# Kernel tuning notes

Measured on AMD Instinct MI355X. Metric: run time of the kernel, lower is better.

Reference implementation:

```python
import jax, jax.numpy as jnp
import numpy as np

G = 4      # deformable groups
K = 9      # 3x3 kernel points
EPS = 1e-5


def _bilinear_gather(value, loc_y, loc_x):
    # value: (N,H,W,G,Cg); loc_*: (N,H,W,G,K) float pixel coords, zero padding outside.
    N, H, W, g, Cg = value.shape
    y0f = jnp.floor(loc_y); x0f = jnp.floor(loc_x)
    wy = loc_y - y0f; wx = loc_x - x0f
    y0 = y0f.astype(jnp.int32); x0 = x0f.astype(jnp.int32)
    n_idx = jnp.arange(N).reshape(N, 1, 1, 1, 1)
    g_idx = jnp.arange(g).reshape(1, 1, 1, g, 1)

    def corner(yi, xi, w):
        valid = (yi >= 0) & (yi < H) & (xi >= 0) & (xi < W)
        yc = jnp.clip(yi, 0, H - 1); xc = jnp.clip(xi, 0, W - 1)
        v = value[n_idx, yc, xc, g_idx]  # (N,H,W,G,K,Cg) irregular gather
        return v * (w * valid)[..., None]

    return (corner(y0, x0, (1 - wy) * (1 - wx))
            + corner(y0, x0 + 1, (1 - wy) * wx)
            + corner(y0 + 1, x0, wy * (1 - wx))
            + corner(y0 + 1, x0 + 1, wy * wx))


def _dcnv4(t, H, W, Wv, bv, Wom, bom, Wo):
    # DCNv4 on (N,L,C): value proj -> learned-offset bilinear sampling with
    # UNNORMALIZED dynamic weights (no softmax, DCNv4) -> output proj (no bias).
    N, L, C = t.shape
    Cg = C // G
    value = (t @ Wv + bv).reshape(N, H, W, G, Cg)
    om = (t @ Wom + bom).reshape(N, H, W, G, 3 * K)
    offset = om[..., :2 * K].reshape(N, H, W, G, K, 2)  # (dx, dy) per point
    mask = om[..., 2 * K:]                               # (N,H,W,G,K)
    ky, kx = jnp.meshgrid(jnp.arange(-1, 2), jnp.arange(-1, 2), indexing='ij')
    ky = ky.reshape(-1).astype(t.dtype); kx = kx.reshape(-1).astype(t.dtype)
    ys = jnp.arange(H, dtype=t.dtype).reshape(1, H, 1, 1, 1)
    xs = jnp.arange(W, dtype=t.dtype).reshape(1, 1, W, 1, 1)
    loc_y = ys + ky + offset[..., 1]  # (N,H,W,G,K)
    loc_x = xs + kx + offset[..., 0]
    sampled = _bilinear_gather(value, loc_y, loc_x)  # (N,H,W,G,K,Cg)
    out = (sampled * mask[..., None]).sum(axis=4)    # (N,H,W,G,Cg)
    return out.reshape(N, L, C) @ Wo


def _bn(x, gamma, beta):
    # training-mode BatchNorm2d: per-channel batch stats over (N,H,W)
    mean = x.mean(axis=(0, 2, 3), keepdims=True)
    var = ((x - mean) ** 2).mean(axis=(0, 2, 3), keepdims=True)
    return (x - mean) * jax.lax.rsqrt(var + EPS) * gamma.reshape(1, -1, 1, 1) \
        + beta.reshape(1, -1, 1, 1)


def setup_inputs() -> dict:
    key = jax.random.key(0)
    ks = jax.random.split(key, 6)
    N, C, H, W = 4, 128, 64, 64
    s = 1.0 / np.sqrt(C)
    x = jax.random.normal(ks[0], (N, C, H, W), jnp.float32)
    Wv = jax.random.normal(ks[1], (C, C), jnp.float32) * s      # value_proj
    bv = jnp.zeros((C,), jnp.float32)
    Wom = jax.random.normal(ks[2], (C, G * 3 * K), jnp.float32) * 0.01  # offset+mask head
    bom = jnp.zeros((G * 3 * K,), jnp.float32)
    Wo = jax.random.normal(ks[3], (C, C), jnp.float32) * s      # output_proj (bias=False)
    gamma = jnp.ones((C,), jnp.float32)
    beta = jnp.zeros((C,), jnp.float32)
    Wc = jax.random.normal(ks[4], (C, C), jnp.float32) * s      # 1x1 conv (out=in=C)
    return {"x": x, "Wv": Wv, "bv": bv, "Wom": Wom, "bom": bom,
            "Wo": Wo, "gamma": gamma, "beta": beta, "Wc": Wc}


def reference(x, Wv, bv, Wom, bom, Wo, gamma, beta, Wc):
    N, C, H, W = x.shape
    shortcut = x
    t = x.transpose(0, 2, 3, 1).reshape(N, H * W, C)
    t = _dcnv4(t, H, W, Wv, bv, Wom, bom, Wo)
    y = t.reshape(N, H, W, C).transpose(0, 3, 1, 2)
    y = jax.nn.relu(_bn(y, gamma, beta))
    t = y.transpose(0, 2, 3, 1).reshape(N, H * W, C)
    t = _dcnv4(t, H, W, Wv, bv, Wom, bom, Wo)  # same DCNv4 weights reused
    y = t.reshape(N, H, W, C).transpose(0, 3, 1, 2)
    y = _bn(y, gamma, beta)                    # same BN params reused, no relu here
    y = y + shortcut                           # in_channels == out_channels
    return jnp.einsum('nchw,oc->nohw', y, Wc)  # final 1x1 conv
```

## Files before the change

kernel.cpp:

```cpp
#include <hip/hip_runtime.h>
#include <math.h>

#define CC   128
#define NL   16384
#define OMP  112
#define HH   64
#define WW   64

typedef __attribute__((ext_vector_type(8))) short short8;
typedef __attribute__((ext_vector_type(4))) float f32x4;

__device__ __forceinline__ unsigned short f2bf(float f) {
    union { float f; unsigned u; } v; v.f = f;
    unsigned r = v.u + 0x7fff + ((v.u >> 16) & 1);
    return (unsigned short)(r >> 16);
}
__device__ __forceinline__ float bf2f(unsigned short u) {
    union { unsigned u; float f; } v; v.u = ((unsigned)u) << 16;
    return v.f;
}

__global__ __launch_bounds__(256) void prep_kernel(
    const float* __restrict__ Wv, const float* __restrict__ Wom,
    const float* __restrict__ Wo, const float* __restrict__ Wc,
    unsigned short* __restrict__ Wcomb, unsigned short* __restrict__ WoT,
    unsigned short* __restrict__ Wcb, float* __restrict__ stats)
{
    int tid = threadIdx.x;
    int b   = blockIdx.x;
    if (b < 16) stats[b * 256 + tid] = 0.0f;
    int i = b * 256 + tid;
    if (i < 32768) {
        int r = i >> 7, k = i & 127;
        unsigned short v;
        if (r < 128)      v = f2bf(Wv[k * CC + r]);
        else if (r < 240) { int nn = r - 128; v = (nn < 108) ? f2bf(Wom[k * 108 + nn]) : (unsigned short)0; }
        else              v = 0;
        Wcomb[i] = v;
    } else if (i < 49152) {
        int j = i - 32768; int nn = j >> 7, k = j & 127;
        WoT[j] = f2bf(Wo[k * CC + nn]);
    } else {
        int j = i - 49152;
        Wcb[j] = f2bf(Wc[j]);
    }
}

template<int IN_MODE>
__global__ __launch_bounds__(256) void gemm_vom_kernel(
    const float* __restrict__ Ain, const unsigned short* __restrict__ Wcomb,
    const float* __restrict__ bv, const float* __restrict__ bom,
    const float* __restrict__ stats, const float* __restrict__ gamma,
    const float* __restrict__ beta,
    unsigned short* __restrict__ val, float* __restrict__ omb)
{
    __shared__ unsigned short As[16 * 136];
    __shared__ float bnsc[128], bnsh[128];

    int tid = threadIdx.x;
    int block_m = blockIdx.x * 16;

    if (IN_MODE == 1) {
        if (tid < 128) {
            float s = 0.0f, sq = 0.0f;
#pragma unroll
            for (int g = 0; g < 8; g++) {
                s  += stats[g * 256 + tid];
                sq += stats[g * 256 + 128 + tid];
            }
            const float inv = 1.0f / 16384.0f;
            float mean = s * inv;
            float var  = sq * inv - mean * mean;
            float sc   = rsqrtf(var + 1e-5f) * gamma[tid];
            bnsc[tid] = sc;
            bnsh[tid] = beta[tid] - mean * sc;
        }
        __syncthreads();
    }

    if (IN_MODE == 0) {
        int n   = block_m >> 12;
        int hw0 = block_m & 4095;
#pragma unroll
        for (int i = 0; i < 2; i++) {
            int id = tid + i * 256;
            int c  = id >> 2, j4 = id & 3;
            float4 v = *(const float4*)(Ain + (((size_t)(n * CC + c)) << 12) + hw0 + j4 * 4);
            As[(j4 * 4 + 0) * 136 + c] = f2bf(v.x);
            As[(j4 * 4 + 1) * 136 + c] = f2bf(v.y);
            As[(j4 * 4 + 2) * 136 + c] = f2bf(v.z);
            As[(j4 * 4 + 3) * 136 + c] = f2bf(v.w);
        }
    } else {
#pragma unroll
        for (int i = 0; i < 2; i++) {
            int id = tid + i * 256;
            int r  = id >> 5, c = (id & 31) * 4;
            float4 v = *(const float4*)(Ain + (size_t)(block_m + r) * CC + c);
            As[r * 136 + c + 0] = f2bf(fmaxf(v.x * bnsc[c + 0] + bnsh[c + 0], 0.0f));
            As[r * 136 + c + 1] = f2bf(fmaxf(v.y * bnsc[c + 1] + bnsh[c + 1], 0.0f));
            As[r * 136 + c + 2] = f2bf(fmaxf(v.z * bnsc[c + 2] + bnsh[c + 2], 0.0f));
            As[r * 136 + c + 3] = f2bf(fmaxf(v.w * bnsc[c + 3] + bnsh[c + 3], 0.0f));
        }
    }
    __syncthreads();

    int w  = tid >> 6;
    int l  = tid & 63;
    int lr = l & 15, lk = l >> 4;

    f32x4 acc[4];
#pragma unroll
    for (int nt = 0; nt < 4; nt++) acc[nt] = (f32x4){0.f, 0.f, 0.f, 0.f};

#pragma unroll
    for (int kk = 0; kk < 4; kk++) {
        short8 a = *(const short8*)(&As[lr * 136 + kk * 32 + lk * 8]);
#pragma unroll
        for (int nt = 0; nt < 4; nt++) {
            int ntile = w + nt * 4;
            short8 b = *(const short8*)(Wcomb + (size_t)(ntile * 16 + lr) * CC + kk * 32 + lk * 8);
            acc[nt] = __builtin_amdgcn_mfma_f32_16x16x32_bf16(a, b, acc[nt], 0, 0, 0);
        }
    }

    int row0 = block_m + lk * 4;
#pragma unroll
    for (int nt = 0; nt < 4; nt++) {
        int col = (w + nt * 4) * 16 + lr;
        if (col < 128) {
            float bb = bv[col];
#pragma unroll
            for (int r = 0; r < 4; r++)
                val[(size_t)(row0 + r) * CC + col] = f2bf(acc[nt][r] + bb);
        } else if (col < 240) {
            int oc = col - 128;
            float bb = (oc < 108) ? bom[oc] : 0.0f;
#pragma unroll
            for (int r = 0; r < 4; r++)
                omb[(size_t)(row0 + r) * OMP + oc] = acc[nt][r] + bb;
        }
    }
}

__global__ __launch_bounds__(256) void sample_kernel(
    const unsigned short* __restrict__ val, const float* __restrict__ omb,
    unsigned int* __restrict__ sbuf)
{
    int tid    = threadIdx.x;
    int gid    = blockIdx.x * 256 + tid;
    int unit   = gid >> 4;
    int lane16 = gid & 15;
    int nl = unit >> 2;
    int g  = unit & 3;
    int n  = nl >> 12;
    int hw = nl & 4095;
    int h  = hw >> 6;
    int w  = hw & 63;

    const float* omp = omb + (size_t)nl * OMP + g * 27;
    const unsigned short* vb = val + (((size_t)n) << 19) + g * 32 + lane16 * 2;

    float acc0 = 0.0f, acc1 = 0.0f;
#pragma unroll
    for (int k = 0; k < 9; k++) {
        float ox = omp[2 * k];
        float oy = omp[2 * k + 1];
        float mk = omp[18 + k];
        float ly = (float)(h + k / 3 - 1) + oy;
        float lx = (float)(w + k % 3 - 1) + ox;
        float y0f = floorf(ly), x0f = floorf(lx);
        float wy = ly - y0f, wx = lx - x0f;
        int y0 = (int)y0f, x0 = (int)x0f;

        float v0 = 0.0f, v1 = 0.0f;
#pragma unroll
        for (int cy = 0; cy < 2; cy++) {
#pragma unroll
            for (int cx = 0; cx < 2; cx++) {
                int yi = y0 + cy, xi = x0 + cx;
                float wgt = (cy ? wy : 1.0f - wy) * (cx ? wx : 1.0f - wx);
                bool valid = (yi >= 0) && (yi < HH) && (xi >= 0) && (xi < WW);
                wgt = valid ? wgt : 0.0f;
                int yc = min(max(yi, 0), HH - 1);
                int xc = min(max(xi, 0), WW - 1);
                unsigned int pv = *(const unsigned int*)(vb + (size_t)(yc * WW + xc) * CC);
                v0 += bf2f((unsigned short)(pv & 0xffff)) * wgt;
                v1 += bf2f((unsigned short)(pv >> 16)) * wgt;
            }
        }
        acc0 += mk * v0;
        acc1 += mk * v1;
    }
    unsigned int packed = (unsigned int)f2bf(acc0) | ((unsigned int)f2bf(acc1) << 16);
    sbuf[(size_t)nl * 64 + g * 16 + lane16] = packed;
}

__global__ __launch_bounds__(256) void gemm_o_bn_kernel(
    const unsigned short* __restrict__ A, const unsigned short* __restrict__ Bt,
    float* __restrict__ ybuf, float* __restrict__ stats)
{
    __shared__ float lstat[256];
    int tid = threadIdx.x;
    int block_m = blockIdx.x * 16;
    lstat[tid] = 0.0f;
    __syncthreads();

    int w  = tid >> 6;
    int l  = tid & 63;
    int lr = l & 15, lk = l >> 4;

    f32x4 acc[2];
    acc[0] = (f32x4){0.f, 0.f, 0.f, 0.f};
    acc[1] = (f32x4){0.f, 0.f, 0.f, 0.f};

#pragma unroll
    for (int kk = 0; kk < 4; kk++) {
        short8 a = *(const short8*)(A + (size_t)(block_m + lr) * CC + kk * 32 + lk * 8);
#pragma unroll
        for (int nt = 0; nt < 2; nt++) {
            short8 b = *(const short8*)(Bt + (size_t)((w * 2 + nt) * 16 + lr) * CC + kk * 32 + lk * 8);
            acc[nt] = __builtin_amdgcn_mfma_f32_16x16x32_bf16(a, b, acc[nt], 0, 0, 0);
        }
    }

    int row0 = block_m + lk * 4;
#pragma unroll
    for (int nt = 0; nt < 2; nt++) {
        int col = (w * 2 + nt) * 16 + lr;
        float s = 0.0f, sq = 0.0f;
#pragma unroll
        for (int r = 0; r < 4; r++) {
            float v = acc[nt][r];
            ybuf[(size_t)(row0 + r) * CC + col] = v;
            s += v;
            sq += v * v;
        }
        atomicAdd(&lstat[col], s);
        atomicAdd(&lstat[128 + col], sq);
    }
    __syncthreads();
    if (tid < 128) {
        float* sg = stats + (blockIdx.x & 7) * 256;
        atomicAdd(&sg[tid], lstat[tid]);
        atomicAdd(&sg[128 + tid], lstat[128 + tid]);
    }
}

__global__ __launch_bounds__(256) void gemm_final_kernel(
    const float* __restrict__ ybuf, const float* __restrict__ x,
    const unsigned short* __restrict__ Bt, const float* __restrict__ stats,
    const float* __restrict__ gamma, const float* __restrict__ beta,
    float* __restrict__ out)
{
    __shared__ unsigned short As[16 * 136];
    __shared__ float Xs[16 * 132];
    __shared__ float T[128 * 20];
    __shared__ float bnsc[128], bnsh[128];

    int tid = threadIdx.x;
    int block_m = blockIdx.x * 16;
    int n   = block_m >> 12;
    int hw0 = block_m & 4095;

    if (tid < 128) {
        float s = 0.0f, sq = 0.0f;
#pragma unroll
        for (int g = 0; g < 8; g++) {
            s  += stats[g * 256 + tid];
            sq += stats[g * 256 + 128 + tid];
        }
        const float inv = 1.0f / 16384.0f;
        float mean = s * inv;
        float var  = sq * inv - mean * mean;
        float sc   = rsqrtf(var + 1e-5f) * gamma[tid];
        bnsc[tid] = sc;
        bnsh[tid] = beta[tid] - mean * sc;
    }

#pragma unroll
    for (int i = 0; i < 2; i++) {
        int id = tid + i * 256;
        int c  = id >> 2, j4 = id & 3;
        float4 v = *(const float4*)(x + (((size_t)(n * CC + c)) << 12) + hw0 + j4 * 4);
        Xs[(j4 * 4 + 0) * 132 + c] = v.x;
        Xs[(j4 * 4 + 1) * 132 + c] = v.y;
        Xs[(j4 * 4 + 2) * 132 + c] = v.z;
        Xs[(j4 * 4 + 3) * 132 + c] = v.w;
    }
    __syncthreads();

#pragma unroll
    for (int i = 0; i < 2; i++) {
        int id = tid + i * 256;
        int r  = id >> 5, c = (id & 31) * 4;
        float4 v = *(const float4*)(ybuf + (size_t)(block_m + r) * CC + c);
        As[r * 136 + c + 0] = f2bf(v.x * bnsc[c + 0] + bnsh[c + 0] + Xs[r * 132 + c + 0]);
        As[r * 136 + c + 1] = f2bf(v.y * bnsc[c + 1] + bnsh[c + 1] + Xs[r * 132 + c + 1]);
        As[r * 136 + c + 2] = f2bf(v.z * bnsc[c + 2] + bnsh[c + 2] + Xs[r * 132 + c + 2]);
        As[r * 136 + c + 3] = f2bf(v.w * bnsc[c + 3] + bnsh[c + 3] + Xs[r * 132 + c + 3]);
    }
    __syncthreads();

    int w  = tid >> 6;
    int l  = tid & 63;
    int lr = l & 15, lk = l >> 4;

    f32x4 acc[2];
    acc[0] = (f32x4){0.f, 0.f, 0.f, 0.f};
    acc[1] = (f32x4){0.f, 0.f, 0.f, 0.f};

#pragma unroll
    for (int kk = 0; kk < 4; kk++) {
        short8 a = *(const short8*)(&As[lr * 136 + kk * 32 + lk * 8]);
#pragma unroll
        for (int nt = 0; nt < 2; nt++) {
            short8 b = *(const short8*)(Bt + (size_t)((w * 2 + nt) * 16 + lr) * CC + kk * 32 + lk * 8);
            acc[nt] = __builtin_amdgcn_mfma_f32_16x16x32_bf16(a, b, acc[nt], 0, 0, 0);
        }
    }

#pragma unroll
    for (int nt = 0; nt < 2; nt++) {
        int col = (w * 2 + nt) * 16 + lr;
#pragma unroll
        for (int r = 0; r < 4; r++)
            T[col * 20 + lk * 4 + r] = acc[nt][r];
    }
    __syncthreads();
#pragma unroll
    for (int i = 0; i < 2; i++) {
        int id = tid + i * 256;
        int o  = id >> 2, j4 = id & 3;
        float4 v = *(const float4*)(&T[o * 20 + j4 * 4]);
        *(float4*)(out + (((size_t)(n * CC + o)) << 12) + hw0 + j4 * 4) = v;
    }
}

extern "C" void kernel_launch(void* const* d_in, const int* in_sizes, int n_in,
                              void* d_out, int out_size, void* d_ws, size_t ws_size,
                              hipStream_t stream)
{
    const float* x     = (const float*)d_in[0];
    const float* Wv    = (const float*)d_in[1];
    const float* bv    = (const float*)d_in[2];
    const float* Wom   = (const float*)d_in[3];
    const float* bom   = (const float*)d_in[4];
    const float* Wo    = (const float*)d_in[5];
    const float* gamma = (const float*)d_in[6];
    const float* beta  = (const float*)d_in[7];
    const float* Wc    = (const float*)d_in[8];
    float* out = (float*)d_out;

    char* ws = (char*)d_ws;
    unsigned short* val   = (unsigned short*)ws;   ws += (size_t)NL * CC * 2;
    float*          omb   = (float*)ws;            ws += (size_t)NL * OMP * 4;
    unsigned int*   sbuf  = (unsigned int*)ws;     ws += (size_t)NL * CC * 2;
    float*          ybuf  = (float*)ws;            ws += (size_t)NL * CC * 4;
    unsigned short* Wcomb = (unsigned short*)ws;   ws += 256 * 128 * 2;
    unsigned short* WoT   = (unsigned short*)ws;   ws += 128 * 128 * 2;
    unsigned short* Wcb   = (unsigned short*)ws;   ws += 128 * 128 * 2;
    float*          stats = (float*)ws;            ws += 4096 * 4;

    dim3 b256(256);

    prep_kernel<<<256, b256, 0, stream>>>(Wv, Wom, Wo, Wc, Wcomb, WoT, Wcb, stats);

    gemm_vom_kernel<0><<<1024, b256, 0, stream>>>(x, Wcomb, bv, bom,
                                                  nullptr, nullptr, nullptr, val, omb);
    sample_kernel<<<4096, b256, 0, stream>>>(val, omb, sbuf);
    gemm_o_bn_kernel<<<1024, b256, 0, stream>>>((const unsigned short*)sbuf, WoT, ybuf, stats);

    gemm_vom_kernel<1><<<1024, b256, 0, stream>>>(ybuf, Wcomb, bv, bom,
                                                  stats, gamma, beta, val, omb);
    sample_kernel<<<4096, b256, 0, stream>>>(val, omb, sbuf);
    gemm_o_bn_kernel<<<1024, b256, 0, stream>>>((const unsigned short*)sbuf, WoT, ybuf, stats + 2048);

    gemm_final_kernel<<<1024, b256, 0, stream>>>(ybuf, x, Wcb, stats + 2048, gamma, beta, out);
}
```

Before: 167.9 us.

## Fuse sampling with output GEMM, enlarge tiles, stage weights in LDS per block

Removes the separate weight-prep kernel: each block now converts Wv/Wom/Wo/Wc to bf16 into shared memory itself. The bilinear sampling kernel is fused with the output projection GEMM and BN statistics, so the intermediate sampled buffer never goes through global memory. Row tiles grow from 16 to 64, cutting the grid to 256 blocks, and each sampling thread now handles 8 channels with 16-byte loads. This saves launches and global traffic, but each block repeats the weight conversion and uses a lot of LDS, which lowers occupancy and parallelism (256 blocks across many CUs).

```diff
diff --git a/kernel.cpp b/kernel.cpp
--- a/kernel.cpp
+++ b/kernel.cpp
@@ -3,7 +3,6 @@
 
 #define CC   128
 #define NL   16384
-#define OMP  112
 #define HH   64
 #define WW   64
 
@@ -20,53 +19,32 @@
     return v.f;
 }
 
-__global__ __launch_bounds__(256) void prep_kernel(
-    const float* __restrict__ Wv, const float* __restrict__ Wom,
-    const float* __restrict__ Wo, const float* __restrict__ Wc,
-    unsigned short* __restrict__ Wcomb, unsigned short* __restrict__ WoT,
-    unsigned short* __restrict__ Wcb, float* __restrict__ stats)
-{
-    int tid = threadIdx.x;
-    int b   = blockIdx.x;
-    if (b < 16) stats[b * 256 + tid] = 0.0f;
-    int i = b * 256 + tid;
-    if (i < 32768) {
-        int r = i >> 7, k = i & 127;
-        unsigned short v;
-        if (r < 128)      v = f2bf(Wv[k * CC + r]);
-        else if (r < 240) { int nn = r - 128; v = (nn < 108) ? f2bf(Wom[k * 108 + nn]) : (unsigned short)0; }
-        else              v = 0;
-        Wcomb[i] = v;
-    } else if (i < 49152) {
-        int j = i - 32768; int nn = j >> 7, k = j & 127;
-        WoT[j] = f2bf(Wo[k * CC + nn]);
-    } else {
-        int j = i - 49152;
-        Wcb[j] = f2bf(Wc[j]);
-    }
-}
-
 template<int IN_MODE>
 __global__ __launch_bounds__(256) void gemm_vom_kernel(
-    const float* __restrict__ Ain, const unsigned short* __restrict__ Wcomb,
-    const float* __restrict__ bv, const float* __restrict__ bom,
-    const float* __restrict__ stats, const float* __restrict__ gamma,
-    const float* __restrict__ beta,
-    unsigned short* __restrict__ val, float* __restrict__ omb)
+    const float* __restrict__ Ain, const float* __restrict__ Wv,
+    const float* __restrict__ bv, const float* __restrict__ Wom,
+    const float* __restrict__ bom, const float* __restrict__ stats_in,
+    const float* __restrict__ gamma, const float* __restrict__ beta,
+    unsigned short* __restrict__ val, float* __restrict__ omb,
+    float* __restrict__ stats_zero)
 {
-    __shared__ unsigned short As[16 * 136];
+    __shared__ unsigned short As[64 * 136];
+    __shared__ unsigned short Bs[128 * 136];
     __shared__ float bnsc[128], bnsh[128];
 
-    int tid = threadIdx.x;
-    int block_m = blockIdx.x * 16;
-
-    if (IN_MODE == 1) {
+    const int tid = threadIdx.x;
+    const int bid = blockIdx.x;
+    const int block_m = bid * 64;
+
+    if (IN_MODE == 0) {
+        if (bid < 16) stats_zero[bid * 256 + tid] = 0.0f;
+    } else {
         if (tid < 128) {
-            float s = 0.0f, sq = 0.0f;
+            float s = 0.f, sq = 0.f;
 #pragma unroll
             for (int g = 0; g < 8; g++) {
-                s  += stats[g * 256 + tid];
-                sq += stats[g * 256 + 128 + tid];
+                s  += stats_in[g * 256 + tid];
+                sq += stats_in[g * 256 + 128 + tid];
             }
             const float inv = 1.0f / 16384.0f;
             float mean = s * inv;
@@ -79,13 +57,13 @@
     }
 
     if (IN_MODE == 0) {
-        int n   = block_m >> 12;
-        int hw0 = block_m & 4095;
-#pragma unroll
-        for (int i = 0; i < 2; i++) {
+        int n_img = block_m >> 12;
+        int hw0   = block_m & 4095;
+#pragma unroll
+        for (int i = 0; i < 8; i++) {
             int id = tid + i * 256;
-            int c  = id >> 2, j4 = id & 3;
-            float4 v = *(const float4*)(Ain + (((size_t)(n * CC + c)) << 12) + hw0 + j4 * 4);
+            int c = id >> 4, j4 = id & 15;
+            float4 v = *(const float4*)(Ain + (((size_t)(n_img * CC + c)) << 12) + hw0 + j4 * 4);
             As[(j4 * 4 + 0) * 136 + c] = f2bf(v.x);
             As[(j4 * 4 + 1) * 136 + c] = f2bf(v.y);
             As[(j4 * 4 + 2) * 136 + c] = f2bf(v.z);
@@ -93,155 +71,237 @@
         }
     } else {
 #pragma unroll
-        for (int i = 0; i < 2; i++) {
+        for (int i = 0; i < 8; i++) {
             int id = tid + i * 256;
-            int r  = id >> 5, c = (id & 31) * 4;
+            int r = id >> 5, c = (id & 31) * 4;
             float4 v = *(const float4*)(Ain + (size_t)(block_m + r) * CC + c);
-            As[r * 136 + c + 0] = f2bf(fmaxf(v.x * bnsc[c + 0] + bnsh[c + 0], 0.0f));
-            As[r * 136 + c + 1] = f2bf(fmaxf(v.y * bnsc[c + 1] + bnsh[c + 1], 0.0f));
-            As[r * 136 + c + 2] = f2bf(fmaxf(v.z * bnsc[c + 2] + bnsh[c + 2], 0.0f));
-            As[r * 136 + c + 3] = f2bf(fmaxf(v.w * bnsc[c + 3] + bnsh[c + 3], 0.0f));
-        }
-    }
-    __syncthreads();
-
-    int w  = tid >> 6;
-    int l  = tid & 63;
-    int lr = l & 15, lk = l >> 4;
-
-    f32x4 acc[4];
-#pragma unroll
-    for (int nt = 0; nt < 4; nt++) acc[nt] = (f32x4){0.f, 0.f, 0.f, 0.f};
-
-#pragma unroll
-    for (int kk = 0; kk < 4; kk++) {
-        short8 a = *(const short8*)(&As[lr * 136 + kk * 32 + lk * 8]);
-#pragma unroll
-        for (int nt = 0; nt < 4; nt++) {
-            int ntile = w + nt * 4;
-            short8 b = *(const short8*)(Wcomb + (size_t)(ntile * 16 + lr) * CC + kk * 32 + lk * 8);
-            acc[nt] = __builtin_amdgcn_mfma_f32_16x16x32_bf16(a, b, acc[nt], 0, 0, 0);
-        }
-    }
-
-    int row0 = block_m + lk * 4;
-#pragma unroll
-    for (int nt = 0; nt < 4; nt++) {
-        int col = (w + nt * 4) * 16 + lr;
-        if (col < 128) {
+            As[r * 136 + c + 0] = f2bf(fmaxf(v.x * bnsc[c + 0] + bnsh[c + 0], 0.f));
+            As[r * 136 + c + 1] = f2bf(fmaxf(v.y * bnsc[c + 1] + bnsh[c + 1], 0.f));
+            As[r * 136 + c + 2] = f2bf(fmaxf(v.z * bnsc[c + 2] + bnsh[c + 2], 0.f));
+            As[r * 136 + c + 3] = f2bf(fmaxf(v.w * bnsc[c + 3] + bnsh[c + 3], 0.f));
+        }
+    }
+#pragma unroll
+    for (int i = 0; i < 16; i++) {
+        int id = tid + i * 256;
+        int k = id >> 5, n4 = (id & 31) * 4;
+        float4 v = *(const float4*)(Wv + (size_t)k * CC + n4);
+        Bs[(n4 + 0) * 136 + k] = f2bf(v.x);
+        Bs[(n4 + 1) * 136 + k] = f2bf(v.y);
+        Bs[(n4 + 2) * 136 + k] = f2bf(v.z);
+        Bs[(n4 + 3) * 136 + k] = f2bf(v.w);
+    }
+    __syncthreads();
+
+    const int w  = tid >> 6;
+    const int l  = tid & 63;
+    const int lr = l & 15;
+    const int lk = l >> 4;
+
+    {
+        f32x4 acc[8];
+#pragma unroll
+        for (int j = 0; j < 8; j++) acc[j] = (f32x4){0.f, 0.f, 0.f, 0.f};
+#pragma unroll
+        for (int kk = 0; kk < 4; kk++) {
+            short8 a = *(const short8*)(&As[(w * 16 + lr) * 136 + kk * 32 + lk * 8]);
+#pragma unroll
+            for (int j = 0; j < 8; j++) {
+                short8 b = *(const short8*)(&Bs[(j * 16 + lr) * 136 + kk * 32 + lk * 8]);
+                acc[j] = __builtin_amdgcn_mfma_f32_16x16x32_bf16(a, b, acc[j], 0, 0, 0);
+            }
+        }
+        int row0 = block_m + w * 16 + lk * 4;
+#pragma unroll
+        for (int j = 0; j < 8; j++) {
+            int col = j * 16 + lr;
             float bb = bv[col];
 #pragma unroll
             for (int r = 0; r < 4; r++)
-                val[(size_t)(row0 + r) * CC + col] = f2bf(acc[nt][r] + bb);
-        } else if (col < 240) {
-            int oc = col - 128;
-            float bb = (oc < 108) ? bom[oc] : 0.0f;
-#pragma unroll
-            for (int r = 0; r < 4; r++)
-                omb[(size_t)(row0 + r) * OMP + oc] = acc[nt][r] + bb;
-        }
-    }
-}
-
-__global__ __launch_bounds__(256) void sample_kernel(
+                val[(size_t)(row0 + r) * CC + col] = f2bf(acc[j][r] + bb);
+        }
+    }
+    __syncthreads();
+
+    if (tid < 68) {
+        int r = 108 + tid / 17, q = tid % 17;
+        float4 z; z.x = 0.f; z.y = 0.f; z.z = 0.f; z.w = 0.f;
+        *(float4*)(&Bs[r * 136 + q * 8]) = z;
+    }
+#pragma unroll
+    for (int i = 0; i < 14; i++) {
+        int id = tid + i * 256;
+        if (id < 3456) {
+            int k = id / 27, q = id - k * 27;
+            float4 v = *(const float4*)(Wom + (size_t)k * 108 + q * 4);
+            Bs[(q * 4 + 0) * 136 + k] = f2bf(v.x);
+            Bs[(q * 4 + 1) * 136 + k] = f2bf(v.y);
+            Bs[(q * 4 + 2) * 136 + k] = f2bf(v.z);
+            Bs[(q * 4 + 3) * 136 + k] = f2bf(v.w);
+        }
+    }
+    __syncthreads();
+
+    {
+        f32x4 acc[7];
+#pragma unroll
+        for (int j = 0; j < 7; j++) acc[j] = (f32x4){0.f, 0.f, 0.f, 0.f};
+#pragma unroll
+        for (int kk = 0; kk < 4; kk++) {
+            short8 a = *(const short8*)(&As[(w * 16 + lr) * 136 + kk * 32 + lk * 8]);
+#pragma unroll
+            for (int j = 0; j < 7; j++) {
+                short8 b = *(const short8*)(&Bs[(j * 16 + lr) * 136 + kk * 32 + lk * 8]);
+                acc[j] = __builtin_amdgcn_mfma_f32_16x16x32_bf16(a, b, acc[j], 0, 0, 0);
+            }
+        }
+        int row0 = block_m + w * 16 + lk * 4;
+#pragma unroll
+        for (int j = 0; j < 7; j++) {
+            int col = j * 16 + lr;
+            if (col < 108) {
+                float bb = bom[col];
+#pragma unroll
+                for (int r = 0; r < 4; r++)
+                    omb[(size_t)(row0 + r) * 112 + col] = acc[j][r] + bb;
+            }
+        }
+    }
+}
+
+__global__ __launch_bounds__(256) void sample_obn_kernel(
     const unsigned short* __restrict__ val, const float* __restrict__ omb,
-    unsigned int* __restrict__ sbuf)
+    const float* __restrict__ Wo, float* __restrict__ ybuf,
+    float* __restrict__ stats_out)
 {
-    int tid    = threadIdx.x;
-    int gid    = blockIdx.x * 256 + tid;
-    int unit   = gid >> 4;
-    int lane16 = gid & 15;
-    int nl = unit >> 2;
-    int g  = unit & 3;
-    int n  = nl >> 12;
-    int hw = nl & 4095;
-    int h  = hw >> 6;
-    int w  = hw & 63;
-
-    const float* omp = omb + (size_t)nl * OMP + g * 27;
-    const unsigned short* vb = val + (((size_t)n) << 19) + g * 32 + lane16 * 2;
-
-    float acc0 = 0.0f, acc1 = 0.0f;
-#pragma unroll
-    for (int k = 0; k < 9; k++) {
-        float ox = omp[2 * k];
-        float oy = omp[2 * k + 1];
-        float mk = omp[18 + k];
-        float ly = (float)(h + k / 3 - 1) + oy;
-        float lx = (float)(w + k % 3 - 1) + ox;
-        float y0f = floorf(ly), x0f = floorf(lx);
-        float wy = ly - y0f, wx = lx - x0f;
-        int y0 = (int)y0f, x0 = (int)x0f;
-
-        float v0 = 0.0f, v1 = 0.0f;
-#pragma unroll
-        for (int cy = 0; cy < 2; cy++) {
-#pragma unroll
-            for (int cx = 0; cx < 2; cx++) {
-                int yi = y0 + cy, xi = x0 + cx;
-                float wgt = (cy ? wy : 1.0f - wy) * (cx ? wx : 1.0f - wx);
-                bool valid = (yi >= 0) && (yi < HH) && (xi >= 0) && (xi < WW);
-                wgt = valid ? wgt : 0.0f;
-                int yc = min(max(yi, 0), HH - 1);
-                int xc = min(max(xi, 0), WW - 1);
-                unsigned int pv = *(const unsigned int*)(vb + (size_t)(yc * WW + xc) * CC);
-                v0 += bf2f((unsigned short)(pv & 0xffff)) * wgt;
-                v1 += bf2f((unsigned short)(pv >> 16)) * wgt;
-            }
-        }
-        acc0 += mk * v0;
-        acc1 += mk * v1;
-    }
-    unsigned int packed = (unsigned int)f2bf(acc0) | ((unsigned int)f2bf(acc1) << 16);
-    sbuf[(size_t)nl * 64 + g * 16 + lane16] = packed;
-}
-
-__global__ __launch_bounds__(256) void gemm_o_bn_kernel(
-    const unsigned short* __restrict__ A, const unsigned short* __restrict__ Bt,
-    float* __restrict__ ybuf, float* __restrict__ stats)
-{
+    __shared__ unsigned short As[64 * 136];
+    __shared__ unsigned short Bs[128 * 136];
+    __shared__ float omtile[64 * 108];
     __shared__ float lstat[256];
-    int tid = threadIdx.x;
-    int block_m = blockIdx.x * 16;
+
+    const int tid = threadIdx.x;
+    const int bid = blockIdx.x;
+    const int block_m = bid * 64;
+    const int n_img = block_m >> 12;
+
     lstat[tid] = 0.0f;
-    __syncthreads();
-
-    int w  = tid >> 6;
-    int l  = tid & 63;
-    int lr = l & 15, lk = l >> 4;
-
-    f32x4 acc[2];
-    acc[0] = (f32x4){0.f, 0.f, 0.f, 0.f};
-    acc[1] = (f32x4){0.f, 0.f, 0.f, 0.f};
-
-#pragma unroll
-    for (int kk = 0; kk < 4; kk++) {
-        short8 a = *(const short8*)(A + (size_t)(block_m + lr) * CC + kk * 32 + lk * 8);
-#pragma unroll
-        for (int nt = 0; nt < 2; nt++) {
-            short8 b = *(const short8*)(Bt + (size_t)((w * 2 + nt) * 16 + lr) * CC + kk * 32 + lk * 8);
-            acc[nt] = __builtin_amdgcn_mfma_f32_16x16x32_bf16(a, b, acc[nt], 0, 0, 0);
-        }
-    }
-
-    int row0 = block_m + lk * 4;
-#pragma unroll
-    for (int nt = 0; nt < 2; nt++) {
-        int col = (w * 2 + nt) * 16 + lr;
-        float s = 0.0f, sq = 0.0f;
-#pragma unroll
-        for (int r = 0; r < 4; r++) {
-            float v = acc[nt][r];
-            ybuf[(size_t)(row0 + r) * CC + col] = v;
-            s += v;
-            sq += v * v;
-        }
-        atomicAdd(&lstat[col], s);
-        atomicAdd(&lstat[128 + col], sq);
+
+#pragma unroll
+    for (int i = 0; i < 7; i++) {
+        int id = tid + i * 256;
+        if (id < 1728) {
+            int r = id / 27, q = id - r * 27;
+            *(float4*)(&omtile[r * 108 + q * 4]) =
+                *(const float4*)(omb + (size_t)(block_m + r) * 112 + q * 4);
+        }
+    }
+#pragma unroll
+    for (int i = 0; i < 16; i++) {
+        int id = tid + i * 256;
+        int k = id >> 5, n4 = (id & 31) * 4;
+        float4 v = *(const float4*)(Wo + (size_t)k * CC + n4);
+        Bs[(n4 + 0) * 136 + k] = f2bf(v.x);
+        Bs[(n4 + 1) * 136 + k] = f2bf(v.y);
+        Bs[(n4 + 2) * 136 + k] = f2bf(v.z);
+        Bs[(n4 + 3) * 136 + k] = f2bf(v.w);
+    }
+    __syncthreads();
+
+    {
+        const unsigned short* vimg = val + (((size_t)n_img) << 19);
+#pragma unroll
+        for (int it = 0; it < 4; it++) {
+            int lane_id = tid + it * 256;
+            int unit = lane_id >> 2;
+            int l4 = lane_id & 3;
+            int r = unit >> 2;
+            int g = unit & 3;
+            int nl = block_m + r;
+            int h  = (nl & 4095) >> 6;
+            int wp = nl & 63;
+            const float* omr = omtile + r * 108 + g * 27;
+            const unsigned short* vb = vimg + g * 32 + l4 * 8;
+
+            float av[8];
+#pragma unroll
+            for (int q = 0; q < 8; q++) av[q] = 0.f;
+#pragma unroll
+            for (int k = 0; k < 9; k++) {
+                float ox = omr[2 * k];
+                float oy = omr[2 * k + 1];
+                float mk = omr[18 + k];
+                float ly = (float)(h + k / 3 - 1) + oy;
+                float lx = (float)(wp + k % 3 - 1) + ox;
+                float y0f = floorf(ly), x0f = floorf(lx);
+                float wy = ly - y0f, wx = lx - x0f;
+                int y0 = (int)y0f, x0 = (int)x0f;
+#pragma unroll
+                for (int cy = 0; cy < 2; cy++) {
+#pragma unroll
+                    for (int cx = 0; cx < 2; cx++) {
+                        int yi = y0 + cy, xi = x0 + cx;
+                        float wgt = (cy ? wy : 1.f - wy) * (cx ? wx : 1.f - wx);
+                        bool valid = (yi >= 0) && (yi < HH) && (xi >= 0) && (xi < WW);
+                        wgt = mk * (valid ? wgt : 0.f);
+                        int yc = min(max(yi, 0), HH - 1);
+                        int xc = min(max(xi, 0), WW - 1);
+                        uint4 pv = *(const uint4*)(vb + (size_t)(yc * WW + xc) * CC);
+                        unsigned pw[4] = {pv.x, pv.y, pv.z, pv.w};
+#pragma unroll
+                        for (int q = 0; q < 4; q++) {
+                            av[2 * q + 0] += bf2f((unsigned short)(pw[q] & 0xffff)) * wgt;
+                            av[2 * q + 1] += bf2f((unsigned short)(pw[q] >> 16)) * wgt;
+                        }
+                    }
+                }
+            }
+            unsigned p0 = (unsigned)f2bf(av[0]) | ((unsigned)f2bf(av[1]) << 16);
+            unsigned p1 = (unsigned)f2bf(av[2]) | ((unsigned)f2bf(av[3]) << 16);
+            unsigned p2 = (unsigned)f2bf(av[4]) | ((unsigned)f2bf(av[5]) << 16);
+            unsigned p3 = (unsigned)f2bf(av[6]) | ((unsigned)f2bf(av[7]) << 16);
+            uint4 pk; pk.x = p0; pk.y = p1; pk.z = p2; pk.w = p3;
+            *(uint4*)(&As[r * 136 + g * 32 + l4 * 8]) = pk;
+        }
+    }
+    __syncthreads();
+
+    const int w  = tid >> 6;
+    const int l  = tid & 63;
+    const int lr = l & 15;
+    const int lk = l >> 4;
+
+    {
+        f32x4 acc[8];
+#pragma unroll
+        for (int j = 0; j < 8; j++) acc[j] = (f32x4){0.f, 0.f, 0.f, 0.f};
+#pragma unroll
+        for (int kk = 0; kk < 4; kk++) {
+            short8 a = *(const short8*)(&As[(w * 16 + lr) * 136 + kk * 32 + lk * 8]);
+#pragma unroll
+            for (int j = 0; j < 8; j++) {
+                short8 b = *(const short8*)(&Bs[(j * 16 + lr) * 136 + kk * 32 + lk * 8]);
+                acc[j] = __builtin_amdgcn_mfma_f32_16x16x32_bf16(a, b, acc[j], 0, 0, 0);
+            }
+        }
+        int row0 = block_m + w * 16 + lk * 4;
+#pragma unroll
+        for (int j = 0; j < 8; j++) {
+            int col = j * 16 + lr;
+            float s = 0.f, sq = 0.f;
+#pragma unroll
+            for (int r = 0; r < 4; r++) {
+                float v = acc[j][r];
+                ybuf[(size_t)(row0 + r) * CC + col] = v;
+                s += v;
+                sq += v * v;
+            }
+            atomicAdd(&lstat[col], s);
+            atomicAdd(&lstat[128 + col], sq);
+        }
     }
     __syncthreads();
     if (tid < 128) {
-        float* sg = stats + (blockIdx.x & 7) * 256;
+        float* sg = stats_out + (bid & 7) * 256;
         atomicAdd(&sg[tid], lstat[tid]);
         atomicAdd(&sg[128 + tid], lstat[128 + tid]);
     }
@@ -249,26 +309,27 @@
 
 __global__ __launch_bounds__(256) void gemm_final_kernel(
     const float* __restrict__ ybuf, const float* __restrict__ x,
-    const unsigned short* __restrict__ Bt, const float* __restrict__ stats,
+    const float* __restrict__ Wc, const float* __restrict__ stats_in,
     const float* __restrict__ gamma, const float* __restrict__ beta,
     float* __restrict__ out)
 {
-    __shared__ unsigned short As[16 * 136];
-    __shared__ float Xs[16 * 132];
-    __shared__ float T[128 * 20];
+    __shared__ unsigned short As[64 * 136];
+    __shared__ unsigned short Bs[128 * 136];
+    __shared__ float Xs[64 * 129];
     __shared__ float bnsc[128], bnsh[128];
-
-    int tid = threadIdx.x;
-    int block_m = blockIdx.x * 16;
-    int n   = block_m >> 12;
-    int hw0 = block_m & 4095;
+    float* Tt = (float*)Bs;
+
+    const int tid = threadIdx.x;
+    const int block_m = blockIdx.x * 64;
+    const int n_img = block_m >> 12;
+    const int hw0 = block_m & 4095;
 
     if (tid < 128) {
-        float s = 0.0f, sq = 0.0f;
+        float s = 0.f, sq = 0.f;
 #pragma unroll
         for (int g = 0; g < 8; g++) {
-            s  += stats[g * 256 + tid];
-            sq += stats[g * 256 + 128 + tid];
+            s  += stats_in[g * 256 + tid];
+            sq += stats_in[g * 256 + 128 + tid];
         }
         const float inv = 1.0f / 16384.0f;
         float mean = s * inv;
@@ -277,63 +338,73 @@
         bnsc[tid] = sc;
         bnsh[tid] = beta[tid] - mean * sc;
     }
-
-#pragma unroll
-    for (int i = 0; i < 2; i++) {
-        int id = tid + i * 256;
-        int c  = id >> 2, j4 = id & 3;
-        float4 v = *(const float4*)(x + (((size_t)(n * CC + c)) << 12) + hw0 + j4 * 4);
-        Xs[(j4 * 4 + 0) * 132 + c] = v.x;
-        Xs[(j4 * 4 + 1) * 132 + c] = v.y;
-        Xs[(j4 * 4 + 2) * 132 + c] = v.z;
-        Xs[(j4 * 4 + 3) * 132 + c] = v.w;
-    }
-    __syncthreads();
-
-#pragma unroll
-    for (int i = 0; i < 2; i++) {
-        int id = tid + i * 256;
-        int r  = id >> 5, c = (id & 31) * 4;
-        float4 v = *(const float4*)(ybuf + (size_t)(block_m + r) * CC + c);
-        As[r * 136 + c + 0] = f2bf(v.x * bnsc[c + 0] + bnsh[c + 0] + Xs[r * 132 + c + 0]);
-        As[r * 136 + c + 1] = f2bf(v.y * bnsc[c + 1] + bnsh[c + 1] + Xs[r * 132 + c + 1]);
-        As[r * 136 + c + 2] = f2bf(v.z * bnsc[c + 2] + bnsh[c + 2] + Xs[r * 132 + c + 2]);
-        As[r * 136 + c + 3] = f2bf(v.w * bnsc[c + 3] + bnsh[c + 3] + Xs[r * 132 + c + 3]);
-    }
-    __syncthreads();
-
-    int w  = tid >> 6;
-    int l  = tid & 63;
-    int lr = l & 15, lk = l >> 4;
-
-    f32x4 acc[2];
-    acc[0] = (f32x4){0.f, 0.f, 0.f, 0.f};
-    acc[1] = (f32x4){0.f, 0.f, 0.f, 0.f};
-
-#pragma unroll
-    for (int kk = 0; kk < 4; kk++) {
-        short8 a = *(const short8*)(&As[lr * 136 + kk * 32 + lk * 8]);
-#pragma unroll
-        for (int nt = 0; nt < 2; nt++) {
-            short8 b = *(const short8*)(Bt + (size_t)((w * 2 + nt) * 16 + lr) * CC + kk * 32 + lk * 8);
-            acc[nt] = __builtin_amdgcn_mfma_f32_16x16x32_bf16(a, b, acc[nt], 0, 0, 0);
-        }
-    }
-
-#pragma unroll
-    for (int nt = 0; nt < 2; nt++) {
-        int col = (w * 2 + nt) * 16 + lr;
-#pragma unroll
-        for (int r = 0; r < 4; r++)
-            T[col * 20 + lk * 4 + r] = acc[nt][r];
-    }
-    __syncthreads();
-#pragma unroll
-    for (int i = 0; i < 2; i++) {
-        int id = tid + i * 256;
-        int o  = id >> 2, j4 = id & 3;
-        float4 v = *(const float4*)(&T[o * 20 + j4 * 4]);
-        *(float4*)(out + (((size_t)(n * CC + o)) << 12) + hw0 + j4 * 4) = v;
+#pragma unroll
+    for (int i = 0; i < 8; i++) {
+        int id = tid + i * 256;
+        int c = id >> 4, j4 = id & 15;
+        float4 v = *(const float4*)(x + (((size_t)(n_img * CC + c)) << 12) + hw0 + j4 * 4);
+        Xs[(j4 * 4 + 0) * 129 + c] = v.x;
+        Xs[(j4 * 4 + 1) * 129 + c] = v.y;
+        Xs[(j4 * 4 + 2) * 129 + c] = v.z;
+        Xs[(j4 * 4 + 3) * 129 + c] = v.w;
+    }
+#pragma unroll
+    for (int i = 0; i < 16; i++) {
+        int id = tid + i * 256;
+        int r = id >> 5, c4 = (id & 31) * 4;
+        float4 v = *(const float4*)(Wc + (size_t)r * CC + c4);
+        Bs[r * 136 + c4 + 0] = f2bf(v.x);
+        Bs[r * 136 + c4 + 1] = f2bf(v.y);
+        Bs[r * 136 + c4 + 2] = f2bf(v.z);
+        Bs[r * 136 + c4 + 3] = f2bf(v.w);
+    }
+    __syncthreads();
+#pragma unroll
+    for (int i = 0; i < 8; i++) {
+        int id = tid + i * 256;
+        int r = id >> 5, c = (id & 31) * 4;
+        float4 yv = *(const float4*)(ybuf + (size_t)(block_m + r) * CC + c);
+        As[r * 136 + c + 0] = f2bf(yv.x * bnsc[c + 0] + bnsh[c + 0] + Xs[r * 129 + c + 0]);
+        As[r * 136 + c + 1] = f2bf(yv.y * bnsc[c + 1] + bnsh[c + 1] + Xs[r * 129 + c + 1]);
+        As[r * 136 + c + 2] = f2bf(yv.z * bnsc[c + 2] + bnsh[c + 2] + Xs[r * 129 + c + 2]);
+        As[r * 136 + c + 3] = f2bf(yv.w * bnsc[c + 3] + bnsh[c + 3] + Xs[r * 129 + c + 3]);
+    }
+    __syncthreads();
+
+    const int w  = tid >> 6;
+    const int l  = tid & 63;
+    const int lr = l & 15;
+    const int lk = l >> 4;
+    {
+        f32x4 acc[8];
+#pragma unroll
+        for (int j = 0; j < 8; j++) acc[j] = (f32x4){0.f, 0.f, 0.f, 0.f};
+#pragma unroll
+        for (int kk = 0; kk < 4; kk++) {
+            short8 a = *(const short8*)(&As[(w * 16 + lr) * 136 + kk * 32 + lk * 8]);
+#pragma unroll
+            for (int j = 0; j < 8; j++) {
+                short8 b = *(const short8*)(&Bs[(j * 16 + lr) * 136 + kk * 32 + lk * 8]);
+                acc[j] = __builtin_amdgcn_mfma_f32_16x16x32_bf16(a, b, acc[j], 0, 0, 0);
+            }
+        }
+        __syncthreads();
+        int row0 = w * 16 + lk * 4;
+#pragma unroll
+        for (int j = 0; j < 8; j++) {
+            int col = j * 16 + lr;
+#pragma unroll
+            for (int r = 0; r < 4; r++)
+                Tt[col * 68 + row0 + r] = acc[j][r];
+        }
+    }
+    __syncthreads();
+#pragma unroll
+    for (int i = 0; i < 8; i++) {
+        int id = tid + i * 256;
+        int o = id >> 4, j4 = id & 15;
+        float4 v = *(const float4*)(&Tt[o * 68 + j4 * 4]);
+        *(float4*)(out + (((size_t)(n_img * CC + o)) << 12) + hw0 + j4 * 4) = v;
     }
 }
 
@@ -341,6 +412,7 @@
                               void* d_out, int out_size, void* d_ws, size_t ws_size,
                               hipStream_t stream)
 {
+    (void)in_sizes; (void)n_in; (void)out_size; (void)ws_size;
     const float* x     = (const float*)d_in[0];
     const float* Wv    = (const float*)d_in[1];
     const float* bv    = (const float*)d_in[2];
@@ -354,27 +426,19 @@
 
     char* ws = (char*)d_ws;
     unsigned short* val   = (unsigned short*)ws;   ws += (size_t)NL * CC * 2;
-    float*          omb   = (float*)ws;            ws += (size_t)NL * OMP * 4;
-    unsigned int*   sbuf  = (unsigned int*)ws;     ws += (size_t)NL * CC * 2;
+    float*          omb   = (float*)ws;            ws += (size_t)NL * 112 * 4;
     float*          ybuf  = (float*)ws;            ws += (size_t)NL * CC * 4;
-    unsigned short* Wcomb = (unsigned short*)ws;   ws += 256 * 128 * 2;
-    unsigned short* WoT   = (unsigned short*)ws;   ws += 128 * 128 * 2;
-    unsigned short* Wcb   = (unsigned short*)ws;   ws += 128 * 128 * 2;
     float*          stats = (float*)ws;            ws += 4096 * 4;
 
     dim3 b256(256);
 
-    prep_kernel<<<256, b256, 0, stream>>>(Wv, Wom, Wo, Wc, Wcomb, WoT, Wcb, stats);
-
-    gemm_vom_kernel<0><<<1024, b256, 0, stream>>>(x, Wcomb, bv, bom,
-                                                  nullptr, nullptr, nullptr, val, omb);
-    sample_kernel<<<4096, b256, 0, stream>>>(val, omb, sbuf);
-    gemm_o_bn_kernel<<<1024, b256, 0, stream>>>((const unsigned short*)sbuf, WoT, ybuf, stats);
-
-    gemm_vom_kernel<1><<<1024, b256, 0, stream>>>(ybuf, Wcomb, bv, bom,
-                                                  stats, gamma, beta, val, omb);
-    sample_kernel<<<4096, b256, 0, stream>>>(val, omb, sbuf);
-    gemm_o_bn_kernel<<<1024, b256, 0, stream>>>((const unsigned short*)sbuf, WoT, ybuf, stats + 2048);
-
-    gemm_final_kernel<<<1024, b256, 0, stream>>>(ybuf, x, Wcb, stats + 2048, gamma, beta, out);
-}
+    gemm_vom_kernel<0><<<256, b256, 0, stream>>>(x, Wv, bv, Wom, bom,
+                                                 nullptr, nullptr, nullptr, val, omb, stats);
+    sample_obn_kernel<<<256, b256, 0, stream>>>(val, omb, Wo, ybuf, stats);
+
+    gemm_vom_kernel<1><<<256, b256, 0, stream>>>(ybuf, Wv, bv, Wom, bom,
+                                                 stats, gamma, beta, val, omb, nullptr);
+    sample_obn_kernel<<<256, b256, 0, stream>>>(val, omb, Wo, ybuf, stats + 2048);
+
+    gemm_final_kernel<<<256, b256, 0, stream>>>(ybuf, x, Wc, stats + 2048, gamma, beta, out);
+}
```

Measured after the change: 157.6 us. 1.07x faster.
